# Kernel tuning notes

Hardware: AMD Instinct MI355X
Metric: run time of the kernel (lower is better)

The kernel has to match this reference:

```python
import jax, jax.numpy as jnp
import numpy as np

NUM_TAGS = 512
START_TAG = 510
STOP_TAG = 511
NEG_INF = -10000.0
BATCH, SEQ_LEN = 64, 512


def setup_inputs() -> dict:
    key = jax.random.key(0)
    k1, k2, k3 = jax.random.split(key, 3)
    inputs = jax.random.normal(k1, (BATCH, SEQ_LEN, NUM_TAGS), dtype=jnp.float32)
    tags = jax.random.randint(k2, (BATCH, SEQ_LEN), 0, 510)
    transitions = jax.random.normal(k3, (NUM_TAGS, NUM_TAGS), dtype=jnp.float32)
    # faithful to __init__: start row and stop column clamped to -10000
    transitions = transitions.at[START_TAG, :].set(NEG_INF).at[:, STOP_TAG].set(NEG_INF)
    return {"inputs": inputs, "tags": tags, "transitions": transitions}


def _lse_source(x):
    # Faithful to the source's log_sum_exp: it subtracts the max but never
    # adds it back, i.e. returns logsumexp(x) - max(x) over the last dim.
    return jax.nn.logsumexp(x, axis=-1) - jnp.max(x, axis=-1)


def _log_denominator(inputs, transitions):
    B, L, T = inputs.shape
    fv0 = jnp.full((B, T), NEG_INF, dtype=inputs.dtype).at[:, START_TAG].set(0.0)

    def step(fv, emit_t):  # fv [B, T_prev], emit_t [B, T_next]
        # scores[b, next, prev] = fv[b, prev] + trans[next, prev] + emit[b, next]
        scores = fv[:, None, :] + transitions[None, :, :] + emit_t[:, :, None]
        return _lse_source(scores), None

    fv, _ = jax.lax.scan(step, fv0, jnp.transpose(inputs, (1, 0, 2)))
    terminal = fv + transitions[STOP_TAG][None, :]
    return _lse_source(terminal)  # [B]


def _log_numerator(inputs, tags, transitions):
    B, L, T = inputs.shape
    score = transitions[tags[:, 0], START_TAG]  # start -> first tag
    # transitions between consecutive tags: trans[tags[:, i+1], tags[:, i]]
    trans_scores = transitions[tags[:, 1:], tags[:, :-1]]  # [B, L-1]
    # emission: faithful to source, uses inputs at position i with tag at i+1
    emit_scores = jnp.take_along_axis(
        inputs[:, :-1, :], tags[:, 1:, None], axis=2
    )[..., 0]  # [B, L-1]
    score = score + jnp.sum(trans_scores + emit_scores, axis=1)
    score = score + transitions[STOP_TAG, tags[:, -1]]
    return score  # [B]


def reference(inputs, tags, transitions):
    log_den = _log_denominator(inputs, transitions)
    log_num = _log_numerator(inputs, tags, transitions)
    return jnp.sum(log_num - log_den)
```

## Files before the change

### kernel.cpp

```cpp
#include <hip/hip_runtime.h>
#include <math.h>
#include <stdint.h>

#define NTAGS 512
#define SEQL  512
#define BATCH 64
#define START_TAG 510
#define STOP_TAG  511
#define NEG_INF  -10000.0f

#define NB   64
#define BT   512
#define ROWS 8
#define REPS 8

#define WS_NUM_OFF  0
#define WS_SLOT_OFF 256
#define WS_BYTES    (WS_SLOT_OFF + 2 * REPS * NTAGS * 8)

#define AGLD(p) __hip_atomic_load((p), __ATOMIC_RELAXED, __HIP_MEMORY_SCOPE_AGENT)

__global__ __launch_bounds__(BT) void crf_fused(
    const float* __restrict__ inputs, const int* __restrict__ tags,
    const float* __restrict__ trans, void* __restrict__ ws,
    float* __restrict__ out)
{
    __shared__ float fv_lds[2][NTAGS];

    const int tid   = threadIdx.x;
    const int bid   = blockIdx.x;
    const int lane  = tid & 63;
    const int wave  = tid >> 6;
    const int myrow = bid * ROWS + wave;
    const int rep   = bid & (REPS - 1);

    float*    numacc = (float*)((char*)ws + WS_NUM_OFF);
    uint64_t* slots  = (uint64_t*)((char*)ws + WS_SLOT_OFF);

    float treg[8];
    {
        const float* trow = trans + (size_t)myrow * NTAGS;
        #pragma unroll
        for (int q = 0; q < 8; ++q) treg[q] = trow[lane + 64 * q];
    }

    float ns;
    {
        const int*   tg  = tags + bid * SEQL;
        const float* inb = inputs + (size_t)bid * SEQL * NTAGS;
        if (tid > 0) {
            const int cur = tg[tid], prev = tg[tid - 1];
            ns = trans[cur * NTAGS + prev] + inb[(size_t)(tid - 1) * NTAGS + cur];
        } else {
            ns = trans[tg[0] * NTAGS + START_TAG] + trans[STOP_TAG * NTAGS + tg[SEQL - 1]];
        }
    }
    #pragma unroll
    for (int off = 32; off; off >>= 1) ns += __shfl_xor(ns, off);
    if (lane == 0) atomicAdd(numacc, ns);
    __builtin_amdgcn_s_waitcnt(0);

    fv_lds[0][tid] = (tid == START_TAG) ? 0.0f : NEG_INF;
    __syncthreads();

    float mprev = (myrow == START_TAG) ? NEG_INF : 0.0f;

    for (int s = 0; s < SEQL; ++s) {
        const int pp = (s + 1) & 1;
        uint64_t* pubbase = slots + (size_t)pp * REPS * NTAGS;
        uint64_t* myslot  = slots + ((size_t)pp * REPS + rep) * NTAGS + tid;
        const unsigned want = (unsigned)(s + 1);
        const float* fvc = fv_lds[s & 1];

        uint64_t p = AGLD(myslot);

        float v[8];
        #pragma unroll
        for (int q = 0; q < 8; ++q)
            v[q] = fvc[lane + 64 * q] + treg[q];

        float m = fmaxf(fmaxf(fmaxf(v[0], v[1]), fmaxf(v[2], v[3])),
                        fmaxf(fmaxf(v[4], v[5]), fmaxf(v[6], v[7])));
        float ss = ((__expf(v[0] - mprev) + __expf(v[1] - mprev))
                  + (__expf(v[2] - mprev) + __expf(v[3] - mprev)))
                 + ((__expf(v[4] - mprev) + __expf(v[5] - mprev))
                  + (__expf(v[6] - mprev) + __expf(v[7] - mprev)));

        #pragma unroll
        for (int off = 32; off; off >>= 1) {
            const float ms  = __shfl_xor(m, off);
            const float sss = __shfl_xor(ss, off);
            m  = fmaxf(m, ms);
            ss += sss;
        }

        {
            const float nv = __logf(ss) + mprev - m;
            const uint64_t pk = ((uint64_t)want << 32) | (uint64_t)__float_as_uint(nv);
            if (lane < REPS)
                __hip_atomic_store(pubbase + (size_t)lane * NTAGS + myrow, pk,
                                   __ATOMIC_RELAXED, __HIP_MEMORY_SCOPE_AGENT);
        }
        mprev = m;

        if ((unsigned)(p >> 32) != want) {
            uint64_t q0 = AGLD(myslot), q1 = AGLD(myslot),
                     q2 = AGLD(myslot), q3 = AGLD(myslot);
            for (;;) {
                if ((unsigned)(q0 >> 32) == want) { p = q0; break; }
                q0 = AGLD(myslot);
                if ((unsigned)(q1 >> 32) == want) { p = q1; break; }
                q1 = AGLD(myslot);
                if ((unsigned)(q2 >> 32) == want) { p = q2; break; }
                q2 = AGLD(myslot);
                if ((unsigned)(q3 >> 32) == want) { p = q3; break; }
                q3 = AGLD(myslot);
            }
        }
        fv_lds[pp][tid] = __uint_as_float((unsigned)(p & 0xFFFFFFFFu));
        __syncthreads();
    }

    if (myrow == STOP_TAG) {
        const float* fvf = fv_lds[0];
        float v[8];
        #pragma unroll
        for (int q = 0; q < 8; ++q)
            v[q] = fvf[lane + 64 * q] + treg[q];
        float m = fmaxf(fmaxf(fmaxf(v[0], v[1]), fmaxf(v[2], v[3])),
                        fmaxf(fmaxf(v[4], v[5]), fmaxf(v[6], v[7])));
        float ss = ((__expf(v[0]) + __expf(v[1])) + (__expf(v[2]) + __expf(v[3])))
                 + ((__expf(v[4]) + __expf(v[5])) + (__expf(v[6]) + __expf(v[7])));
        #pragma unroll
        for (int off = 32; off; off >>= 1) {
            const float ms  = __shfl_xor(m, off);
            const float sss = __shfl_xor(ss, off);
            m  = fmaxf(m, ms);
            ss += sss;
        }
        if (lane == 0) {
            const float ld  = __logf(ss) - m;
            const float num = AGLD(numacc);
            out[0] = num - (float)BATCH * ld;
        }
    }
}

extern "C" void kernel_launch(void* const* d_in, const int* in_sizes, int n_in,
                              void* d_out, int out_size, void* d_ws, size_t ws_size,
                              hipStream_t stream)
{
    const float* inputs = (const float*)d_in[0];
    const int*   tags   = (const int*)  d_in[1];
    const float* trans  = (const float*)d_in[2];
    float* out = (float*)d_out;

    hipMemsetAsync(d_ws, 0, WS_BYTES, stream);

    crf_fused<<<NB, BT, 0, stream>>>(inputs, tags, trans, d_ws, out);
}
```

Baseline: 829.4 us.

## Move CRF forward recursion to linear domain with per-step publish buffers

The recursion now runs in the exponential (linear) domain. Transitions are pre-exponentiated once, so each step is a multiply, a sum and a max followed by one divide, with no per-element exp/log. The ping-pong 64-bit versioned slots and the LDS staging with __syncthreads are replaced by a separate 32-bit buffer per timestep, zero-initialised so that a nonzero value means ready. Each wave then reads the published vector straight into registers. The cost is a much larger workspace and memset, and it relies on published values never being exactly zero (underflow risk), with reps reduced when the workspace is too small.

```diff
diff --git a/kernel.cpp b/kernel.cpp
--- a/kernel.cpp
+++ b/kernel.cpp
@@ -12,36 +12,53 @@
 #define NB   64
 #define BT   512
 #define ROWS 8
-#define REPS 8
+#define MAXREPS 8
 
 #define WS_NUM_OFF  0
 #define WS_SLOT_OFF 256
-#define WS_BYTES    (WS_SLOT_OFF + 2 * REPS * NTAGS * 8)
 
-#define AGLD(p) __hip_atomic_load((p), __ATOMIC_RELAXED, __HIP_MEMORY_SCOPE_AGENT)
+#define AGLD(p)   __hip_atomic_load((p),      __ATOMIC_RELAXED, __HIP_MEMORY_SCOPE_AGENT)
+#define AGST(p,v) __hip_atomic_store((p),(v), __ATOMIC_RELAXED, __HIP_MEMORY_SCOPE_AGENT)
+
+__device__ __forceinline__ void rowreduce(const float wv[8], const float treg[8],
+                                          float& sp, float& mq)
+{
+    float t[8];
+    #pragma unroll
+    for (int q = 0; q < 8; ++q) t[q] = wv[q] * treg[q];
+    sp = ((t[0] + t[1]) + (t[2] + t[3])) + ((t[4] + t[5]) + (t[6] + t[7]));
+    mq = fmaxf(fmaxf(fmaxf(t[0], t[1]), fmaxf(t[2], t[3])),
+               fmaxf(fmaxf(t[4], t[5]), fmaxf(t[6], t[7])));
+    #pragma unroll
+    for (int off = 32; off; off >>= 1) {
+        const float ms = __shfl_xor(mq, off);
+        const float ss = __shfl_xor(sp, off);
+        mq = fmaxf(mq, ms);
+        sp += ss;
+    }
+}
 
 __global__ __launch_bounds__(BT) void crf_fused(
     const float* __restrict__ inputs, const int* __restrict__ tags,
     const float* __restrict__ trans, void* __restrict__ ws,
-    float* __restrict__ out)
+    float* __restrict__ out, const int reps)
 {
-    __shared__ float fv_lds[2][NTAGS];
-
     const int tid   = threadIdx.x;
     const int bid   = blockIdx.x;
     const int lane  = tid & 63;
     const int wave  = tid >> 6;
     const int myrow = bid * ROWS + wave;
-    const int rep   = bid & (REPS - 1);
+    const int rep   = bid & (reps - 1);
 
     float*    numacc = (float*)((char*)ws + WS_NUM_OFF);
-    uint64_t* slots  = (uint64_t*)((char*)ws + WS_SLOT_OFF);
+    uint32_t* slots  = (uint32_t*)((char*)ws + WS_SLOT_OFF);
 
     float treg[8];
     {
-        const float* trow = trans + (size_t)myrow * NTAGS;
+        const float* trow  = trans + (size_t)myrow * NTAGS;
+        const float  shift = (myrow == START_TAG) ? -NEG_INF : 0.0f;
         #pragma unroll
-        for (int q = 0; q < 8; ++q) treg[q] = trow[lane + 64 * q];
+        for (int q = 0; q < 8; ++q) treg[q] = __expf(trow[lane + 64 * q] + shift);
     }
 
     float ns;
@@ -60,86 +77,42 @@
     if (lane == 0) atomicAdd(numacc, ns);
     __builtin_amdgcn_s_waitcnt(0);
 
-    fv_lds[0][tid] = (tid == START_TAG) ? 0.0f : NEG_INF;
-    __syncthreads();
+    float wv[8];
+    #pragma unroll
+    for (int q = 0; q < 8; ++q) wv[q] = ((lane + 64 * q) == START_TAG) ? 1.0f : 0.0f;
 
-    float mprev = (myrow == START_TAG) ? NEG_INF : 0.0f;
+    const size_t lvl_stride = (size_t)reps * NTAGS;
 
     for (int s = 0; s < SEQL; ++s) {
-        const int pp = (s + 1) & 1;
-        uint64_t* pubbase = slots + (size_t)pp * REPS * NTAGS;
-        uint64_t* myslot  = slots + ((size_t)pp * REPS + rep) * NTAGS + tid;
-        const unsigned want = (unsigned)(s + 1);
-        const float* fvc = fv_lds[s & 1];
+        float sp, mq;
+        rowreduce(wv, treg, sp, mq);
+        const float wn = __fdividef(sp, mq);
 
-        uint64_t p = AGLD(myslot);
+        const size_t base = (size_t)(s + 1) * lvl_stride;
 
-        float v[8];
+        if (lane < reps)
+            AGST(slots + base + (size_t)lane * NTAGS + myrow, __float_as_uint(wn));
+
+        const uint32_t* pl = slots + base + (size_t)rep * NTAGS + lane;
+        uint32_t g[8];
         #pragma unroll
-        for (int q = 0; q < 8; ++q)
-            v[q] = fvc[lane + 64 * q] + treg[q];
-
-        float m = fmaxf(fmaxf(fmaxf(v[0], v[1]), fmaxf(v[2], v[3])),
-                        fmaxf(fmaxf(v[4], v[5]), fmaxf(v[6], v[7])));
-        float ss = ((__expf(v[0] - mprev) + __expf(v[1] - mprev))
-                  + (__expf(v[2] - mprev) + __expf(v[3] - mprev)))
-                 + ((__expf(v[4] - mprev) + __expf(v[5] - mprev))
-                  + (__expf(v[6] - mprev) + __expf(v[7] - mprev)));
-
+        for (int q = 0; q < 8; ++q) g[q] = AGLD(pl + 64 * q);
+        for (;;) {
+            bool miss = false;
+            #pragma unroll
+            for (int q = 0; q < 8; ++q)
+                if (g[q] == 0u) { g[q] = AGLD(pl + 64 * q); miss = true; }
+            if (!__any(miss)) break;
+        }
         #pragma unroll
-        for (int off = 32; off; off >>= 1) {
-            const float ms  = __shfl_xor(m, off);
-            const float sss = __shfl_xor(ss, off);
-            m  = fmaxf(m, ms);
-            ss += sss;
-        }
-
-        {
-            const float nv = __logf(ss) + mprev - m;
-            const uint64_t pk = ((uint64_t)want << 32) | (uint64_t)__float_as_uint(nv);
-            if (lane < REPS)
-                __hip_atomic_store(pubbase + (size_t)lane * NTAGS + myrow, pk,
-                                   __ATOMIC_RELAXED, __HIP_MEMORY_SCOPE_AGENT);
-        }
-        mprev = m;
-
-        if ((unsigned)(p >> 32) != want) {
-            uint64_t q0 = AGLD(myslot), q1 = AGLD(myslot),
-                     q2 = AGLD(myslot), q3 = AGLD(myslot);
-            for (;;) {
-                if ((unsigned)(q0 >> 32) == want) { p = q0; break; }
-                q0 = AGLD(myslot);
-                if ((unsigned)(q1 >> 32) == want) { p = q1; break; }
-                q1 = AGLD(myslot);
-                if ((unsigned)(q2 >> 32) == want) { p = q2; break; }
-                q2 = AGLD(myslot);
-                if ((unsigned)(q3 >> 32) == want) { p = q3; break; }
-                q3 = AGLD(myslot);
-            }
-        }
-        fv_lds[pp][tid] = __uint_as_float((unsigned)(p & 0xFFFFFFFFu));
-        __syncthreads();
+        for (int q = 0; q < 8; ++q) wv[q] = __uint_as_float(g[q]);
     }
 
     if (myrow == STOP_TAG) {
-        const float* fvf = fv_lds[0];
-        float v[8];
-        #pragma unroll
-        for (int q = 0; q < 8; ++q)
-            v[q] = fvf[lane + 64 * q] + treg[q];
-        float m = fmaxf(fmaxf(fmaxf(v[0], v[1]), fmaxf(v[2], v[3])),
-                        fmaxf(fmaxf(v[4], v[5]), fmaxf(v[6], v[7])));
-        float ss = ((__expf(v[0]) + __expf(v[1])) + (__expf(v[2]) + __expf(v[3])))
-                 + ((__expf(v[4]) + __expf(v[5])) + (__expf(v[6]) + __expf(v[7])));
-        #pragma unroll
-        for (int off = 32; off; off >>= 1) {
-            const float ms  = __shfl_xor(m, off);
-            const float sss = __shfl_xor(ss, off);
-            m  = fmaxf(m, ms);
-            ss += sss;
-        }
+        float sp, mq;
+        rowreduce(wv, treg, sp, mq);
         if (lane == 0) {
-            const float ld  = __logf(ss) - m;
+            const float ld  = __logf(sp) - __logf(mq);
             const float num = AGLD(numacc);
             out[0] = num - (float)BATCH * ld;
         }
@@ -155,7 +128,13 @@
     const float* trans  = (const float*)d_in[2];
     float* out = (float*)d_out;
 
-    hipMemsetAsync(d_ws, 0, WS_BYTES, stream);
+    int reps = MAXREPS;
+    auto need = [](int r) {
+        return (size_t)WS_SLOT_OFF + (size_t)(SEQL + 1) * (size_t)r * NTAGS * sizeof(uint32_t);
+    };
+    while (reps > 1 && need(reps) > ws_size) reps >>= 1;
 
-    crf_fused<<<NB, BT, 0, stream>>>(inputs, tags, trans, d_ws, out);
+    hipMemsetAsync(d_ws, 0, need(reps), stream);
+
+    crf_fused<<<NB, BT, 0, stream>>>(inputs, tags, trans, d_ws, out, reps);
 }
```

After: 2.348 ms. 2.83x slower.
